# Kernel tuning notes

Hardware: AMD Instinct MI355X
Metric: run time of the kernel (lower is better)

Reference implementation:

```python
import jax, jax.numpy as jnp
import numpy as np

N_NODES = 50000
N_EDGES = 800000
D_IN, D_H, D_Z = 128, 128, 64


def setup_inputs() -> dict:
    key = jax.random.key(0)
    k0, k1, k2, k3, k4 = jax.random.split(key, 5)
    x = jax.random.normal(k0, (N_NODES, D_IN), dtype=jnp.float32)
    edge_index = jax.random.randint(k1, (2, N_EDGES), 0, N_NODES)
    # SAGEConv fc_neigh weights (out_feats, in_feats), bias=False
    W1 = jax.random.normal(k2, (D_H, D_IN), dtype=jnp.float32) / np.sqrt(D_IN)
    W2 = jax.random.normal(k3, (D_H, D_H), dtype=jnp.float32) / np.sqrt(D_H)
    W3 = jax.random.normal(k4, (D_Z, D_H), dtype=jnp.float32) / np.sqrt(D_H)
    return {"x": x, "edge_index": edge_index, "W1": W1, "W2": W2, "W3": W3}


def reference(x, edge_index, W1, W2, W3):
    src, dst = edge_index[0], edge_index[1]
    n = x.shape[0]
    # 'gcn' aggregator: (sum of neighbor feats + self feat) / (in_degree + 1)
    deg = jax.ops.segment_sum(jnp.ones((src.shape[0],), dtype=x.dtype), dst,
                              num_segments=n)
    inv = 1.0 / (deg + 1.0)  # [N]

    def sage_gcn(h, W):
        agg = jax.ops.segment_sum(h[src], dst, num_segments=n) + h  # [N, d_in]
        return (agg * inv[:, None]) @ W.T  # [N, d_out]

    # dropout=0 -> identity; batchnorm in the original is applied to x and
    # discarded, so it never affects h.
    h = jax.nn.relu(sage_gcn(x, W1))
    h = jax.nn.relu(sage_gcn(h, W2))
    h = sage_gcn(h, W3)
    return jax.nn.relu(h)
```

## Files before the change

kernel.cpp:

```cpp
#include <hip/hip_runtime.h>

#define N_NODES 50000
#define N_EDGES 800000
#define D 128


__global__ void deg_kernel(const int* __restrict__ dst, int* __restrict__ deg) {
  int e = blockIdx.x * 256 + threadIdx.x;
  if (e < N_EDGES) atomicAdd(&deg[dst[e]], 1);
}

__global__ void scan_kernel(const int* __restrict__ deg, int* __restrict__ row_start,
                            float* __restrict__ inv) {
  __shared__ int wsum[16];
  __shared__ int carry_s;
  const int t = threadIdx.x;
  const int lane = t & 63, wid = t >> 6;
  if (t == 0) carry_s = 0;
  __syncthreads();
  for (int base = 0; base < N_NODES; base += 4096) {
    int i0 = base + t * 4;
    int v[4];
    int s = 0;
#pragma unroll
    for (int j = 0; j < 4; ++j) {
      int i = i0 + j;
      v[j] = (i < N_NODES) ? deg[i] : 0;
      s += v[j];
    }
    int run = s;
#pragma unroll
    for (int off = 1; off < 64; off <<= 1) {
      int o = __shfl_up(run, off);
      if (lane >= off) run += o;
    }
    if (lane == 63) wsum[wid] = run;
    __syncthreads();
    if (t < 16) {
      int w = wsum[t];
#pragma unroll
      for (int off = 1; off < 16; off <<= 1) {
        int o = __shfl_up(w, off, 16);
        if (t >= off) w += o;
      }
      wsum[t] = w;
    }
    __syncthreads();
    int excl = carry_s + (wid ? wsum[wid - 1] : 0) + run - s;
#pragma unroll
    for (int j = 0; j < 4; ++j) {
      int i = i0 + j;
      if (i < N_NODES) {
        row_start[i] = excl;
        inv[i] = 1.0f / (float)(v[j] + 1);
      }
      excl += v[j];
    }
    __syncthreads();
    if (t == 0) carry_s += wsum[15];
    __syncthreads();
  }
  if (t == 0) row_start[N_NODES] = carry_s;
}

__global__ void csr_kernel(const int* __restrict__ src, const int* __restrict__ dst,
                           const int* __restrict__ row_start, int* __restrict__ cursor,
                           int* __restrict__ csr) {
  int e = blockIdx.x * 256 + threadIdx.x;
  if (e < N_EDGES) {
    int d = dst[e];
    int p = atomicAdd(&cursor[d], 1);
    csr[row_start[d] + p] = src[e];
  }
}

__global__ void wtrans_kernel(const float* __restrict__ W1, const float* __restrict__ W2,
                              const float* __restrict__ W3, float* __restrict__ wT) {
  int g = blockIdx.x * 256 + threadIdx.x;
  if (g < 16384) {
    int k = g >> 7, o = g & 127;
    wT[g] = W1[o * 128 + k];
  } else if (g < 32768) {
    int l = g - 16384;
    int k = l >> 7, o = l & 127;
    wT[g] = W2[o * 128 + k];
  } else if (g < 40960) {
    int l = g - 32768;
    int k = l >> 6, o = l & 63;
    wT[g] = W3[o * 128 + k];
  }
}


template <int DV, bool RELU>
__global__ __launch_bounds__(256) void agg_kernel(const float* __restrict__ G,
    const int* __restrict__ row_start, const int* __restrict__ csr,
    const float* __restrict__ inv, float* __restrict__ outA) {
  constexpr int L = DV / 4;
  constexpr int NPW = 64 / L;
  const int wave = (blockIdx.x * 256 + threadIdx.x) >> 6;
  const int lane = threadIdx.x & 63;
  const int sub = lane / L;
  const int li = lane % L;
  const int node = wave * NPW + sub;

  const float4* hp = (const float4*)G;
  float4 acc = hp[(size_t)node * L + li];
  const int s = row_start[node], e = row_start[node + 1];
  int j = s;
  for (; j + 4 <= e; j += 4) {
    int n0 = csr[j + 0], n1 = csr[j + 1], n2 = csr[j + 2], n3 = csr[j + 3];
    float4 v0 = hp[(size_t)n0 * L + li];
    float4 v1 = hp[(size_t)n1 * L + li];
    float4 v2 = hp[(size_t)n2 * L + li];
    float4 v3 = hp[(size_t)n3 * L + li];
    acc.x += (v0.x + v1.x) + (v2.x + v3.x);
    acc.y += (v0.y + v1.y) + (v2.y + v3.y);
    acc.z += (v0.z + v1.z) + (v2.z + v3.z);
    acc.w += (v0.w + v1.w) + (v2.w + v3.w);
  }
  for (; j < e; ++j) {
    int nb = csr[j];
    float4 v = hp[(size_t)nb * L + li];
    acc.x += v.x; acc.y += v.y; acc.z += v.z; acc.w += v.w;
  }
  float iv = inv[node];
  acc.x *= iv; acc.y *= iv; acc.z *= iv; acc.w *= iv;
  if (RELU) {
    acc.x = fmaxf(acc.x, 0.f); acc.y = fmaxf(acc.y, 0.f);
    acc.z = fmaxf(acc.z, 0.f); acc.w = fmaxf(acc.w, 0.f);
  }
  ((float4*)outA)[(size_t)node * L + li] = acc;
}

template <int DOUT>
__global__ __launch_bounds__(256) void gemm_kernel(const float* __restrict__ A,
    const float* __restrict__ wT, float* __restrict__ out) {
  __shared__ float aL[64 * 128];
  __shared__ float wL[128 * 64];
  const int t = threadIdx.x;
  const int row0 = blockIdx.x * 64;
  const int ob = blockIdx.y * 64;

  {
    const float4* A4 = (const float4*)A;
#pragma unroll
    for (int i = 0; i < 8; ++i) {
      int g4 = t + i * 256;
      int r = g4 >> 5;
      int k4 = g4 & 31;
      int gr = row0 + r;
      float4 v = make_float4(0.f, 0.f, 0.f, 0.f);
      if (gr < N_NODES) v = A4[(size_t)gr * 32 + k4];
      int col = (k4 << 2) ^ (((r >> 3) & 7) << 2);
      *(float4*)&aL[r * 128 + col] = v;
    }
    const float4* w4 = (const float4*)wT;
#pragma unroll
    for (int i = 0; i < 8; ++i) {
      int g4 = t + i * 256;
      int k = g4 >> 4;
      int o4 = g4 & 15;
      float4 v = w4[k * (DOUT / 4) + (ob >> 2) + o4];
      *(float4*)&wL[k * 64 + (o4 << 2)] = v;
    }
  }
  __syncthreads();

  const int rowT = t >> 4, outT = t & 15;
  const int r0 = rowT * 4, o0 = outT * 4;
  const int swz = ((rowT >> 1) & 7) << 2;
  float acc[4][4];
#pragma unroll
  for (int i = 0; i < 4; ++i)
#pragma unroll
    for (int j = 0; j < 4; ++j) acc[i][j] = 0.f;

#pragma unroll 4
  for (int k = 0; k < 128; ++k) {
    int kc = k ^ swz;
    float a0 = aL[(r0 + 0) * 128 + kc];
    float a1 = aL[(r0 + 1) * 128 + kc];
    float a2 = aL[(r0 + 2) * 128 + kc];
    float a3 = aL[(r0 + 3) * 128 + kc];
    float4 b = *(const float4*)&wL[k * 64 + o0];
    acc[0][0] += a0 * b.x; acc[0][1] += a0 * b.y; acc[0][2] += a0 * b.z; acc[0][3] += a0 * b.w;
    acc[1][0] += a1 * b.x; acc[1][1] += a1 * b.y; acc[1][2] += a1 * b.z; acc[1][3] += a1 * b.w;
    acc[2][0] += a2 * b.x; acc[2][1] += a2 * b.y; acc[2][2] += a2 * b.z; acc[2][3] += a2 * b.w;
    acc[3][0] += a3 * b.x; acc[3][1] += a3 * b.y; acc[3][2] += a3 * b.z; acc[3][3] += a3 * b.w;
  }

#pragma unroll
  for (int i = 0; i < 4; ++i) {
    int gr = row0 + r0 + i;
    if (gr < N_NODES) {
      float4 v = make_float4(acc[i][0], acc[i][1], acc[i][2], acc[i][3]);
      *(float4*)&out[(size_t)gr * DOUT + ob + o0] = v;
    }
  }
}


extern "C" void kernel_launch(void* const* d_in, const int* in_sizes, int n_in,
                              void* d_out, int out_size, void* d_ws, size_t ws_size,
                              hipStream_t stream) {
  const float* x  = (const float*)d_in[0];
  const int* ei   = (const int*)d_in[1];
  const float* W1 = (const float*)d_in[2];
  const float* W2 = (const float*)d_in[3];
  const float* W3 = (const float*)d_in[4];
  const int* src = ei;
  const int* dst = ei + N_EDGES;
  float* out = (float*)d_out;

  char* ws = (char*)d_ws;
  size_t off = 0;
  auto alloc = [&](size_t bytes) {
    void* p = ws + off;
    off += (bytes + 255) & ~(size_t)255;
    return p;
  };
  int* deg       = (int*)alloc(N_NODES * sizeof(int));
  int* row_start = (int*)alloc((N_NODES + 1) * sizeof(int));
  int* cursor    = (int*)alloc(N_NODES * sizeof(int));
  int* csr       = (int*)alloc(N_EDGES * sizeof(int));
  float* inv     = (float*)alloc(N_NODES * sizeof(float));
  float* wT      = (float*)alloc((16384 + 16384 + 8192) * sizeof(float));
  float* G       = (float*)alloc((size_t)N_NODES * D * sizeof(float));
  float* H       = (float*)alloc((size_t)N_NODES * D * sizeof(float));
  (void)ws_size;

  float* wT1 = wT;
  float* wT2 = wT + 16384;
  float* wT3 = wT + 32768;

  hipMemsetAsync(deg, 0, N_NODES * sizeof(int), stream);
  hipMemsetAsync(cursor, 0, N_NODES * sizeof(int), stream);

  const int eblocks = (N_EDGES + 255) / 256;
  deg_kernel<<<eblocks, 256, 0, stream>>>(dst, deg);
  scan_kernel<<<1, 1024, 0, stream>>>(deg, row_start, inv);
  csr_kernel<<<eblocks, 256, 0, stream>>>(src, dst, row_start, cursor, csr);
  wtrans_kernel<<<(40960 + 255) / 256, 256, 0, stream>>>(W1, W2, W3, wT);

  const int gblocks = (N_NODES + 63) / 64;

  gemm_kernel<128><<<dim3(gblocks, 2), 256, 0, stream>>>(x, wT1, G);
  agg_kernel<128, true><<<6250, 256, 0, stream>>>(G, row_start, csr, inv, H);
  gemm_kernel<128><<<dim3(gblocks, 2), 256, 0, stream>>>(H, wT2, G);
  agg_kernel<128, true><<<6250, 256, 0, stream>>>(G, row_start, csr, inv, H);
  gemm_kernel<64><<<dim3(gblocks, 1), 256, 0, stream>>>(H, wT3, G);
  agg_kernel<64, true><<<3125, 256, 0, stream>>>(G, row_start, csr, inv, out);
}
```

Before: 461.2 us.

## Seed CSR cursors in scan, unroll aggregation by eight, vectorize GEMM LDS reads

```diff
diff --git a/kernel.cpp b/kernel.cpp
--- a/kernel.cpp
+++ b/kernel.cpp
@@ -11,7 +11,7 @@
 }
 
 __global__ void scan_kernel(const int* __restrict__ deg, int* __restrict__ row_start,
-                            float* __restrict__ inv) {
+                            int* __restrict__ cursor, float* __restrict__ inv) {
   __shared__ int wsum[16];
   __shared__ int carry_s;
   const int t = threadIdx.x;
@@ -52,6 +52,7 @@
       int i = i0 + j;
       if (i < N_NODES) {
         row_start[i] = excl;
+        cursor[i] = excl;
         inv[i] = 1.0f / (float)(v[j] + 1);
       }
       excl += v[j];
@@ -64,13 +65,11 @@
 }
 
 __global__ void csr_kernel(const int* __restrict__ src, const int* __restrict__ dst,
-                           const int* __restrict__ row_start, int* __restrict__ cursor,
-                           int* __restrict__ csr) {
+                           int* __restrict__ cursor, int* __restrict__ csr) {
   int e = blockIdx.x * 256 + threadIdx.x;
   if (e < N_EDGES) {
-    int d = dst[e];
-    int p = atomicAdd(&cursor[d], 1);
-    csr[row_start[d] + p] = src[e];
+    int p = atomicAdd(&cursor[dst[e]], 1);
+    csr[p] = src[e];
   }
 }
 
@@ -106,8 +105,29 @@
 
   const float4* hp = (const float4*)G;
   float4 acc = hp[(size_t)node * L + li];
+  float4 acc2 = make_float4(0.f, 0.f, 0.f, 0.f);
   const int s = row_start[node], e = row_start[node + 1];
   int j = s;
+  for (; j + 8 <= e; j += 8) {
+    int n0 = csr[j + 0], n1 = csr[j + 1], n2 = csr[j + 2], n3 = csr[j + 3];
+    int n4 = csr[j + 4], n5 = csr[j + 5], n6 = csr[j + 6], n7 = csr[j + 7];
+    float4 v0 = hp[(size_t)n0 * L + li];
+    float4 v1 = hp[(size_t)n1 * L + li];
+    float4 v2 = hp[(size_t)n2 * L + li];
+    float4 v3 = hp[(size_t)n3 * L + li];
+    float4 v4 = hp[(size_t)n4 * L + li];
+    float4 v5 = hp[(size_t)n5 * L + li];
+    float4 v6 = hp[(size_t)n6 * L + li];
+    float4 v7 = hp[(size_t)n7 * L + li];
+    acc.x  += (v0.x + v1.x) + (v2.x + v3.x);
+    acc.y  += (v0.y + v1.y) + (v2.y + v3.y);
+    acc.z  += (v0.z + v1.z) + (v2.z + v3.z);
+    acc.w  += (v0.w + v1.w) + (v2.w + v3.w);
+    acc2.x += (v4.x + v5.x) + (v6.x + v7.x);
+    acc2.y += (v4.y + v5.y) + (v6.y + v7.y);
+    acc2.z += (v4.z + v5.z) + (v6.z + v7.z);
+    acc2.w += (v4.w + v5.w) + (v6.w + v7.w);
+  }
   for (; j + 4 <= e; j += 4) {
     int n0 = csr[j + 0], n1 = csr[j + 1], n2 = csr[j + 2], n3 = csr[j + 3];
     float4 v0 = hp[(size_t)n0 * L + li];
@@ -122,8 +142,9 @@
   for (; j < e; ++j) {
     int nb = csr[j];
     float4 v = hp[(size_t)nb * L + li];
-    acc.x += v.x; acc.y += v.y; acc.z += v.z; acc.w += v.w;
-  }
+    acc2.x += v.x; acc2.y += v.y; acc2.z += v.z; acc2.w += v.w;
+  }
+  acc.x += acc2.x; acc.y += acc2.y; acc.z += acc2.z; acc.w += acc2.w;
   float iv = inv[node];
   acc.x *= iv; acc.y *= iv; acc.z *= iv; acc.w *= iv;
   if (RELU) {
@@ -134,7 +155,7 @@
 }
 
 template <int DOUT>
-__global__ __launch_bounds__(256) void gemm_kernel(const float* __restrict__ A,
+__global__ __launch_bounds__(256, 2) void gemm_kernel(const float* __restrict__ A,
     const float* __restrict__ wT, float* __restrict__ out) {
   __shared__ float aL[64 * 128];
   __shared__ float wL[128 * 64];
@@ -144,32 +165,33 @@
 
   {
     const float4* A4 = (const float4*)A;
+    float4* aL4 = (float4*)aL;
 #pragma unroll
     for (int i = 0; i < 8; ++i) {
       int g4 = t + i * 256;
       int r = g4 >> 5;
-      int k4 = g4 & 31;
+      int kb = g4 & 31;
       int gr = row0 + r;
       float4 v = make_float4(0.f, 0.f, 0.f, 0.f);
-      if (gr < N_NODES) v = A4[(size_t)gr * 32 + k4];
-      int col = (k4 << 2) ^ (((r >> 3) & 7) << 2);
-      *(float4*)&aL[r * 128 + col] = v;
+      if (gr < N_NODES) v = A4[(size_t)gr * 32 + kb];
+      aL4[r * 32 + (kb ^ (r & 7))] = v;
     }
     const float4* w4 = (const float4*)wT;
+    float4* wL4 = (float4*)wL;
 #pragma unroll
     for (int i = 0; i < 8; ++i) {
       int g4 = t + i * 256;
       int k = g4 >> 4;
       int o4 = g4 & 15;
-      float4 v = w4[k * (DOUT / 4) + (ob >> 2) + o4];
-      *(float4*)&wL[k * 64 + (o4 << 2)] = v;
+      wL4[k * 16 + o4] = w4[k * (DOUT / 4) + (ob >> 2) + o4];
     }
   }
   __syncthreads();
 
   const int rowT = t >> 4, outT = t & 15;
-  const int r0 = rowT * 4, o0 = outT * 4;
-  const int swz = ((rowT >> 1) & 7) << 2;
+  const int r0 = rowT * 4;
+  const float4* aL4 = (const float4*)aL;
+  const float4* wL4 = (const float4*)wL;
   float acc[4][4];
 #pragma unroll
   for (int i = 0; i < 4; ++i)
@@ -177,17 +199,22 @@
     for (int j = 0; j < 4; ++j) acc[i][j] = 0.f;
 
 #pragma unroll 4
-  for (int k = 0; k < 128; ++k) {
-    int kc = k ^ swz;
-    float a0 = aL[(r0 + 0) * 128 + kc];
-    float a1 = aL[(r0 + 1) * 128 + kc];
-    float a2 = aL[(r0 + 2) * 128 + kc];
-    float a3 = aL[(r0 + 3) * 128 + kc];
-    float4 b = *(const float4*)&wL[k * 64 + o0];
-    acc[0][0] += a0 * b.x; acc[0][1] += a0 * b.y; acc[0][2] += a0 * b.z; acc[0][3] += a0 * b.w;
-    acc[1][0] += a1 * b.x; acc[1][1] += a1 * b.y; acc[1][2] += a1 * b.z; acc[1][3] += a1 * b.w;
-    acc[2][0] += a2 * b.x; acc[2][1] += a2 * b.y; acc[2][2] += a2 * b.z; acc[2][3] += a2 * b.w;
-    acc[3][0] += a3 * b.x; acc[3][1] += a3 * b.y; acc[3][2] += a3 * b.z; acc[3][3] += a3 * b.w;
+  for (int kb = 0; kb < 32; ++kb) {
+    float4 a[4];
+#pragma unroll
+    for (int i = 0; i < 4; ++i) a[i] = aL4[(r0 + i) * 32 + (kb ^ ((r0 + i) & 7))];
+#pragma unroll
+    for (int j = 0; j < 4; ++j) {
+      float4 b = wL4[(kb * 4 + j) * 16 + outT];
+      float a0 = ((const float*)&a[0])[j];
+      float a1 = ((const float*)&a[1])[j];
+      float a2 = ((const float*)&a[2])[j];
+      float a3 = ((const float*)&a[3])[j];
+      acc[0][0] += a0 * b.x; acc[0][1] += a0 * b.y; acc[0][2] += a0 * b.z; acc[0][3] += a0 * b.w;
+      acc[1][0] += a1 * b.x; acc[1][1] += a1 * b.y; acc[1][2] += a1 * b.z; acc[1][3] += a1 * b.w;
+      acc[2][0] += a2 * b.x; acc[2][1] += a2 * b.y; acc[2][2] += a2 * b.z; acc[2][3] += a2 * b.w;
+      acc[3][0] += a3 * b.x; acc[3][1] += a3 * b.y; acc[3][2] += a3 * b.z; acc[3][3] += a3 * b.w;
+    }
   }
 
 #pragma unroll
@@ -195,7 +222,7 @@
     int gr = row0 + r0 + i;
     if (gr < N_NODES) {
       float4 v = make_float4(acc[i][0], acc[i][1], acc[i][2], acc[i][3]);
-      *(float4*)&out[(size_t)gr * DOUT + ob + o0] = v;
+      *(float4*)&out[(size_t)gr * DOUT + ob + (outT << 2)] = v;
     }
   }
 }
@@ -235,12 +262,11 @@
   float* wT3 = wT + 32768;
 
   hipMemsetAsync(deg, 0, N_NODES * sizeof(int), stream);
-  hipMemsetAsync(cursor, 0, N_NODES * sizeof(int), stream);
 
   const int eblocks = (N_EDGES + 255) / 256;
   deg_kernel<<<eblocks, 256, 0, stream>>>(dst, deg);
-  scan_kernel<<<1, 1024, 0, stream>>>(deg, row_start, inv);
-  csr_kernel<<<eblocks, 256, 0, stream>>>(src, dst, row_start, cursor, csr);
+  scan_kernel<<<1, 1024, 0, stream>>>(deg, row_start, cursor, inv);
+  csr_kernel<<<eblocks, 256, 0, stream>>>(src, dst, cursor, csr);
   wtrans_kernel<<<(40960 + 255) / 256, 256, 0, stream>>>(W1, W2, W3, wT);
 
   const int gblocks = (N_NODES + 63) / 64;
```

New measurement: 451.2 us. 1.02x faster.
